# Optimization experiments

Hardware: AMD Instinct MI355X
Metric: run time of the kernel (lower is better)

## Reference

```python
import jax, jax.numpy as jnp
import numpy as np

B, S, D, H, K = 2, 1024, 1024, 16, 33  # batch, seq, d_model, heads, rel buckets (k+1)
d = D // H


def setup_inputs() -> dict:
    key = jax.random.key(0)
    ks = jax.random.split(key, 16)
    w = lambda k, shape: jax.random.normal(k, shape, dtype=jnp.float32) * 0.02
    return {
        "hidden_state": jax.random.normal(ks[0], (B, S, D), dtype=jnp.float32),
        "pos_indices": jax.random.randint(ks[1], (B, S, S), 0, K),
        "mask": jax.random.bernoulli(ks[2], 0.1, (B, 1, 1, S)),
        "Wq": w(ks[3], (D, D)), "bq": w(ks[4], (D,)),
        "Wk": w(ks[5], (D, D)), "bk": w(ks[6], (D,)),
        "Wv": w(ks[7], (D, D)), "bv": w(ks[8], (D,)),
        "Wo": w(ks[9], (D, D)), "bo": w(ks[10], (D,)),
        "rel_q": w(ks[11], (H, K, d)),
        "rel_k": w(ks[12], (H, K, d)),
        "rel_v": w(ks[13], (H, K, d)),
    }


def reference(hidden_state, pos_indices, mask, Wq, bq, Wk, bk, Wv, bv, Wo, bo,
              rel_q, rel_k, rel_v):
    b, s, dm = hidden_state.shape
    h, k_, dp = rel_q.shape
    # projections -> [B,H,S,d]
    def proj(x, W, bias):
        return (x @ W + bias).reshape(b, s, h, dp).transpose(0, 2, 1, 3)
    q = proj(hidden_state, Wq, bq)
    kk = proj(hidden_state, Wk, bk)
    v = proj(hidden_state, Wv, bv)
    # scale_factor = 1 (c2c) + 1 (rel_q) + 1 (rel_k)
    scale = 1.0 / np.sqrt(dp * 3).astype(np.float32)
    # content-to-content
    c2c = jnp.einsum("bhid,bhjd->bhij", q, kk) * scale
    idx = jnp.broadcast_to(pos_indices[:, None], (b, h, s, s))
    # position-to-content: raw [B,H,K,S], gathered along K with per-(i,j) bucket
    raw_p2c = jnp.einsum("hkd,bhjd->bhkj", rel_q, kk) * scale
    p2c = jnp.take_along_axis(raw_p2c, idx, axis=2)
    # content-to-position: raw [B,H,S,K], gathered along K
    raw_c2p = jnp.einsum("bhid,hkd->bhik", q, rel_k) * scale
    c2p = jnp.take_along_axis(raw_c2p, idx, axis=3)
    scores = c2c + p2c + c2p
    scores = jnp.where(mask, jnp.float32(-1e9), scores)
    probs = jax.nn.softmax(scores, axis=-1)  # dropout is identity in eval
    ctx = jnp.einsum("bhij,bhjd->bhid", probs, v)
    # value-side relative term: sum_j P[i,j] * rel_v[bucket(i,j)]
    oh = jax.nn.one_hot(pos_indices, k_, dtype=probs.dtype)  # [B,S,S,K]
    agg = jnp.einsum("bhij,bijk->bhik", probs, oh)
    ctx = ctx + jnp.einsum("bhik,hkd->bhid", agg, rel_v)
    out = ctx.transpose(0, 2, 1, 3).reshape(b, s, dm)
    return out @ Wo + bo
```

## Files before the change

### kernel.cpp

```cpp
#include <hip/hip_runtime.h>
#include <hip/hip_bf16.h>

#define B_ 2
#define S_ 1024
#define D_ 1024
#define H_ 16
#define K_ 33
#define DH 64
#define SCALE 0.07216878364870322f
#define FXS 32768.0f
#define FXI (1.0f / 32768.0f)

typedef __attribute__((ext_vector_type(8))) short bf16x8;
typedef __attribute__((ext_vector_type(4))) float f32x4;

__device__ __forceinline__ float b2f(unsigned short u) {
    return __uint_as_float(((unsigned int)u) << 16);
}
__device__ __forceinline__ unsigned short f2b(float f) {
    unsigned int u = __float_as_uint(f);
    u += 0x7FFFu + ((u >> 16) & 1u);
    return (unsigned short)(u >> 16);
}
__device__ __forceinline__ float ldf(const void* p, int i, int f32) {
    return f32 ? ((const float*)p)[i] : b2f(((const unsigned short*)p)[i]);
}
__device__ __forceinline__ float4 ldf4(const void* p, int i, int f32) {
    if (f32) return *(const float4*)((const float*)p + i);
    ushort4 u = *(const ushort4*)((const unsigned short*)p + i);
    return make_float4(b2f(u.x), b2f(u.y), b2f(u.z), b2f(u.w));
}
__device__ __forceinline__ float4 ldb4(const unsigned short* p, int i) {
    ushort4 u = *(const ushort4*)(p + i);
    return make_float4(b2f(u.x), b2f(u.y), b2f(u.z), b2f(u.w));
}

__global__ __launch_bounds__(256) void prep(const void* __restrict__ hidden,
                                            const void* __restrict__ mask,
                                            int* __restrict__ flags,
                                            float* __restrict__ mflag) {
    __shared__ int cnt;
    __shared__ int mev[6];
    const int t = threadIdx.x;
    if (t == 0) cnt = 0;
    if (t < 6) mev[t] = 0;
    __syncthreads();
    const unsigned short* hu = (const unsigned short*)hidden;
    int c = 0;
    for (int i = t; i < 2048; i += 256) {
        int e = (hu[i] >> 7) & 0xFF;
        if (e >= 0x8E) c++;
    }
    if (c) atomicAdd(&cnt, c);
    const unsigned char* mb = (const unsigned char*)mask;
    int e_bf = 0, e_f32 = 0, e_f64 = 0, e_f16 = 0, e_u8 = 0;
    for (int p = t; p < 2048; p += 256) {
        unsigned char v = mb[p];
        if ((p & 7) == 6 && v == 0xF0) e_f64 = 1;
        if ((p & 3) == 1 && v == 0x3F) e_bf = 1;
        if ((p & 3) == 3 && v == 0x3F) e_f32 = 1;
        if ((p & 1) == 1 && v == 0x3C) e_f16 = 1;
        if ((p & 3) != 0 && v != 0) e_u8 = 1;
    }
    if (e_f64) atomicOr(&mev[5], 1);
    if (e_bf)  atomicOr(&mev[3], 1);
    if (e_f32) atomicOr(&mev[2], 1);
    if (e_f16) atomicOr(&mev[4], 1);
    if (e_u8)  atomicOr(&mev[1], 1);
    __syncthreads();
    const int f32flag = (cnt >= 8) ? 1 : 0;
    const int mm = mev[5] ? 5 : (mev[3] ? 3 : (mev[2] ? 2 : (mev[4] ? 4 : (mev[1] ? 1 : 0))));
    if (t == 0) { flags[0] = f32flag; flags[2] = mm; }
    for (int j = t; j < B_ * S_; j += 256) {
        int m;
        if (mm == 5)      m = (((const double*)mask)[j] != 0.0);
        else if (mm == 3 || mm == 4) m = (((const unsigned short*)mask)[j] != 0);
        else if (mm == 2) m = (((const float*)mask)[j] != 0.f);
        else if (mm == 1) m = (mb[j] != 0);
        else              m = (((const int*)mask)[j] != 0);
        mflag[j] = m ? 1.f : 0.f;
    }
}

__global__ __launch_bounds__(256) void pos_pack(const int* __restrict__ pos,
                                                unsigned char* __restrict__ pos8) {
    int i = blockIdx.x * 256 + threadIdx.x;
    if (i >= (B_ * S_ * S_) / 4) return;
    int4 p = *(const int4*)&pos[i * 4];
    uchar4 o;
    o.x = (unsigned char)min(max(p.x, 0), K_ - 1);
    o.y = (unsigned char)min(max(p.y, 0), K_ - 1);
    o.z = (unsigned char)min(max(p.z, 0), K_ - 1);
    o.w = (unsigned char)min(max(p.w, 0), K_ - 1);
    *(uchar4*)&pos8[i * 4] = o;
}

__global__ __launch_bounds__(256) void w_pack(const void* __restrict__ W0,
                                              const void* __restrict__ W1,
                                              const void* __restrict__ W2,
                                              const void* __restrict__ W3,
                                              const int* __restrict__ flags,
                                              unsigned short* __restrict__ T0,
                                              unsigned short* __restrict__ T1,
                                              unsigned short* __restrict__ T2,
                                              unsigned short* __restrict__ T3) {
    __shared__ unsigned short tl[64][66];
    const int f32u = flags[0];
    const int z = blockIdx.z;
    const void* W = z == 0 ? W0 : (z == 1 ? W1 : (z == 2 ? W2 : W3));
    unsigned short* T = z == 0 ? T0 : (z == 1 ? T1 : (z == 2 ? T2 : T3));
    const int k0 = blockIdx.y * 64, n0 = blockIdx.x * 64;
    const int t = threadIdx.x;
    {
        int kr = t >> 2, nc = (t & 3) * 16;
#pragma unroll
        for (int u = 0; u < 4; ++u) {
            float4 v = ldf4(W, (k0 + kr) * 1024 + n0 + nc + u * 4, f32u);
            tl[kr][nc + u * 4 + 0] = f2b(v.x);
            tl[kr][nc + u * 4 + 1] = f2b(v.y);
            tl[kr][nc + u * 4 + 2] = f2b(v.z);
            tl[kr][nc + u * 4 + 3] = f2b(v.w);
        }
    }
    __syncthreads();
    {
        int nr = t >> 2, kc = (t & 3) * 16;
        unsigned short o[16];
#pragma unroll
        for (int u = 0; u < 16; ++u) o[u] = tl[kc + u][nr];
#pragma unroll
        for (int u = 0; u < 4; ++u)
            *(ushort4*)&T[(n0 + nr) * 1024 + k0 + kc + u * 4] = *(ushort4*)&o[u * 4];
    }
}

__global__ __launch_bounds__(512, 2) void gemm_qkv_mfma(const void* __restrict__ X,
                                                        const void* __restrict__ W0,
                                                        const void* __restrict__ W1,
                                                        const void* __restrict__ W2,
                                                        const unsigned short* __restrict__ T0,
                                                        const unsigned short* __restrict__ T1,
                                                        const unsigned short* __restrict__ T2,
                                                        const void* __restrict__ b0,
                                                        const void* __restrict__ b1,
                                                        const void* __restrict__ b2,
                                                        const int* __restrict__ flags, int useT,
                                                        unsigned short* __restrict__ q,
                                                        unsigned short* __restrict__ kk_,
                                                        unsigned short* __restrict__ v) {
    __shared__ unsigned short Asl[128][40];
    __shared__ unsigned short Bsl[128][40];
    const int f32u = flags[0];
    const int z = blockIdx.z;
    const void* W = z == 0 ? W0 : (z == 1 ? W1 : W2);
    const unsigned short* WT = z == 0 ? T0 : (z == 1 ? T1 : T2);
    const void* bias = z == 0 ? b0 : (z == 1 ? b1 : b2);
    unsigned short* outp = z == 0 ? q : (z == 1 ? kk_ : v);
    const int m0 = blockIdx.y * 128, n0 = blockIdx.x * 128;
    const int t = threadIdx.x;
    const int w = t >> 6, lane = t & 63;
    const int wr = w >> 2, wc = w & 3;
    const int lm = lane & 15, lg = lane >> 4;

    const int am = t >> 2, ac8 = (t & 3) * 8;
    const int bn = t & 127, bkq = (t >> 7) * 8;

    f32x4 acc[4][2] = {};
    float4 pa0, pa1;
    ushort4 tb0, tb1;
    float pbx[8];

    {
        int base = (m0 + am) * 1024 + ac8;
        pa0 = ldf4(X, base, f32u);
        pa1 = ldf4(X, base + 4, f32u);
        if (useT) {
            const ushort4* s = (const ushort4*)&WT[(n0 + am) * 1024 + ac8];
            tb0 = s[0]; tb1 = s[1];
        } else {
#pragma unroll
            for (int qi = 0; qi < 8; ++qi)
                pbx[qi] = ldf(W, (bkq + qi) * 1024 + n0 + bn, f32u);
        }
    }

    for (int k0 = 0; k0 < 1024; k0 += 32) {
        {
            ushort4 u0 = {f2b(pa0.x), f2b(pa0.y), f2b(pa0.z), f2b(pa0.w)};
            ushort4 u1 = {f2b(pa1.x), f2b(pa1.y), f2b(pa1.z), f2b(pa1.w)};
            *(ushort4*)&Asl[am][ac8] = u0;
            *(ushort4*)&Asl[am][ac8 + 4] = u1;
            if (useT) {
                *(ushort4*)&Bsl[am][ac8] = tb0;
                *(ushort4*)&Bsl[am][ac8 + 4] = tb1;
            } else {
#pragma unroll
                for (int qi = 0; qi < 8; qi += 2) {
                    unsigned int pk = (unsigned int)f2b(pbx[qi]) |
                                      ((unsigned int)f2b(pbx[qi + 1]) << 16);
                    *(unsigned int*)&Bsl[bn][bkq + qi] = pk;
                }
            }
        }
        __syncthreads();
        if (k0 + 32 < 1024) {
            int kn = k0 + 32;
            int base = (m0 + am) * 1024 + kn + ac8;
            pa0 = ldf4(X, base, f32u);
            pa1 = ldf4(X, base + 4, f32u);
            if (useT) {
                const ushort4* s = (const ushort4*)&WT[(n0 + am) * 1024 + kn + ac8];
                tb0 = s[0]; tb1 = s[1];
            } else {
#pragma unroll
                for (int qi = 0; qi < 8; ++qi)
                    pbx[qi] = ldf(W, (kn + bkq + qi) * 1024 + n0 + bn, f32u);
            }
        }
        bf16x8 af[4], bfr[2];
#pragma unroll
        for (int mi = 0; mi < 4; ++mi)
            af[mi] = *(const bf16x8*)&Asl[wr * 64 + mi * 16 + lm][lg * 8];
#pragma unroll
        for (int nj = 0; nj < 2; ++nj)
            bfr[nj] = *(const bf16x8*)&Bsl[wc * 32 + nj * 16 + lm][lg * 8];
#pragma unroll
        for (int mi = 0; mi < 4; ++mi)
#pragma unroll
            for (int nj = 0; nj < 2; ++nj)
                acc[mi][nj] = __builtin_amdgcn_mfma_f32_16x16x32_bf16(af[mi], bfr[nj],
                                                                      acc[mi][nj], 0, 0, 0);
        __syncthreads();
    }
#pragma unroll
    for (int nj = 0; nj < 2; ++nj) {
        int n = n0 + wc * 32 + nj * 16 + lm;
        float bv = ldf(bias, n, f32u);
        int hh = n >> 6, dd = n & 63;
#pragma unroll
        for (int mi = 0; mi < 4; ++mi) {
#pragma unroll
            for (int r = 0; r < 4; ++r) {
                int m = m0 + wr * 64 + mi * 16 + lg * 4 + r;
                int bb = m >> 10, ii = m & 1023;
                outp[((bb * H_ + hh) * S_ + ii) * DH + dd] = f2b(acc[mi][nj][r] + bv);
            }
        }
    }
}

__global__ __launch_bounds__(512, 2) void gemm_out_mfma(const unsigned short* __restrict__ X,
                                                        const void* __restrict__ W,
                                                        const unsigned short* __restrict__ WT,
                                                        const void* __restrict__ bias,
                                                        const int* __restrict__ flags, int useT,
                                                        float* __restrict__ out) {
    __shared__ unsigned short Asl[128][40];
    __shared__ unsigned short Bsl[128][40];
    const int f32u = flags[0];
    const int m0 = blockIdx.y * 128, n0 = blockIdx.x * 128;
    const int t = threadIdx.x;
    const int w = t >> 6, lane = t & 63;
    const int wr = w >> 2, wc = w & 3;
    const int lm = lane & 15, lg = lane >> 4;

    const int am = t >> 2, ac8 = (t & 3) * 8;
    const int bn = t & 127, bkq = (t >> 7) * 8;

    f32x4 acc[4][2] = {};
    ushort4 pa0, pa1, tb0, tb1;
    float pbx[8];

    {
        const ushort4* src = (const ushort4*)&X[(m0 + am) * 1024 + ac8];
        pa0 = src[0];
        pa1 = src[1];
        if (useT) {
            const ushort4* s = (const ushort4*)&WT[(n0 + am) * 1024 + ac8];
            tb0 = s[0]; tb1 = s[1];
        } else {
#pragma unroll
            for (int qi = 0; qi < 8; ++qi)
                pbx[qi] = ldf(W, (bkq + qi) * 1024 + n0 + bn, f32u);
        }
    }

    for (int k0 = 0; k0 < 1024; k0 += 32) {
        {
            *(ushort4*)&Asl[am][ac8] = pa0;
            *(ushort4*)&Asl[am][ac8 + 4] = pa1;
            if (useT) {
                *(ushort4*)&Bsl[am][ac8] = tb0;
                *(ushort4*)&Bsl[am][ac8 + 4] = tb1;
            } else {
#pragma unroll
                for (int qi = 0; qi < 8; qi += 2) {
                    unsigned int pk = (unsigned int)f2b(pbx[qi]) |
                                      ((unsigned int)f2b(pbx[qi + 1]) << 16);
                    *(unsigned int*)&Bsl[bn][bkq + qi] = pk;
                }
            }
        }
        __syncthreads();
        if (k0 + 32 < 1024) {
            int kn = k0 + 32;
            const ushort4* src = (const ushort4*)&X[(m0 + am) * 1024 + kn + ac8];
            pa0 = src[0];
            pa1 = src[1];
            if (useT) {
                const ushort4* s = (const ushort4*)&WT[(n0 + am) * 1024 + kn + ac8];
                tb0 = s[0]; tb1 = s[1];
            } else {
#pragma unroll
                for (int qi = 0; qi < 8; ++qi)
                    pbx[qi] = ldf(W, (kn + bkq + qi) * 1024 + n0 + bn, f32u);
            }
        }
        bf16x8 af[4], bfr[2];
#pragma unroll
        for (int mi = 0; mi < 4; ++mi)
            af[mi] = *(const bf16x8*)&Asl[wr * 64 + mi * 16 + lm][lg * 8];
#pragma unroll
        for (int nj = 0; nj < 2; ++nj)
            bfr[nj] = *(const bf16x8*)&Bsl[wc * 32 + nj * 16 + lm][lg * 8];
#pragma unroll
        for (int mi = 0; mi < 4; ++mi)
#pragma unroll
            for (int nj = 0; nj < 2; ++nj)
                acc[mi][nj] = __builtin_amdgcn_mfma_f32_16x16x32_bf16(af[mi], bfr[nj],
                                                                      acc[mi][nj], 0, 0, 0);
        __syncthreads();
    }
#pragma unroll
    for (int nj = 0; nj < 2; ++nj) {
        int n = n0 + wc * 32 + nj * 16 + lm;
        float bv = ldf(bias, n, f32u);
#pragma unroll
        for (int mi = 0; mi < 4; ++mi) {
#pragma unroll
            for (int r = 0; r < 4; ++r) {
                int m = m0 + wr * 64 + mi * 16 + lg * 4 + r;
                out[m * 1024 + n] = acc[mi][nj][r] + bv;
            }
        }
    }
}

__global__ __launch_bounds__(256) void rel_fused(const unsigned short* __restrict__ kws,
                                                 const unsigned short* __restrict__ qws,
                                                 const void* __restrict__ relq,
                                                 const void* __restrict__ relk,
                                                 const int* __restrict__ flags,
                                                 unsigned short* __restrict__ p2c,
                                                 unsigned short* __restrict__ c2p) {
    __shared__ float xt[64][68];
    __shared__ float rr[33][68];
    const int f32u = flags[0];
    const int bh = blockIdx.y, h = bh & 15;
    const int x0 = blockIdx.x * 64;
    const int t = threadIdx.x;
    if (blockIdx.z == 0) {
#pragma unroll
        for (int qq = 0; qq < 4; ++qq) {
            int idx = t + 256 * qq;
            int j = idx >> 4, d4 = idx & 15;
            *(float4*)&xt[j][d4 * 4] = ldb4(kws, (bh * S_ + x0 + j) * DH + d4 * 4);
        }
        for (int idx = t; idx < 33 * 16; idx += 256) {
            int k = idx >> 4, d4 = idx & 15;
            *(float4*)&rr[k][d4 * 4] = ldf4(relq, (h * K_ + k) * DH + d4 * 4, f32u);
        }
        __syncthreads();
        for (int o = t; o < 33 * 64; o += 256) {
            int k = o >> 6, j = o & 63;
            float s = 0.f;
#pragma unroll
            for (int d4 = 0; d4 < 16; ++d4) {
                float4 a = *(const float4*)&rr[k][d4 * 4];
                float4 b = *(const float4*)&xt[j][d4 * 4];
                s += a.x * b.x + a.y * b.y + a.z * b.z + a.w * b.w;
            }
            p2c[(bh * K_ + k) * S_ + x0 + j] = f2b(s * SCALE);
        }
    } else {
#pragma unroll
        for (int qq = 0; qq < 4; ++qq) {
            int idx = t + 256 * qq;
            int i = idx >> 4, d4 = idx & 15;
            *(float4*)&xt[i][d4 * 4] = ldb4(qws, (bh * S_ + x0 + i) * DH + d4 * 4);
        }
        for (int idx = t; idx < 33 * 16; idx += 256) {
            int k = idx >> 4, d4 = idx & 15;
            *(float4*)&rr[k][d4 * 4] = ldf4(relk, (h * K_ + k) * DH + d4 * 4, f32u);
        }
        __syncthreads();
        for (int o = t; o < 64 * 33; o += 256) {
            int i = o / 33, k = o % 33;
            float s = 0.f;
#pragma unroll
            for (int d4 = 0; d4 < 16; ++d4) {
                float4 a = *(const float4*)&xt[i][d4 * 4];
                float4 b = *(const float4*)&rr[k][d4 * 4];
                s += a.x * b.x + a.y * b.y + a.z * b.z + a.w * b.w;
            }
            c2p[(bh * S_ + x0 + i) * K_ + k] = f2b(s * SCALE);
        }
    }
}

#define PS_OFF   0
#define VT_OFF   32768
#define P2CS_OFF 32768
#define C2P_OFF  50176
#define AG_OFF   54528
#define RV_OFF   63232
#define MF_OFF   67456
#define ATTN_LDS 68480

__device__ __forceinline__ int ps_addr(int il, int jc) {
    return PS_OFF + il * 512 +
           ((jc * 2) ^ ((((il >> 2) & 3) << 5) ^ ((il & 3) << 4)));
}

__global__ __launch_bounds__(512, 4) void attn_mfma(const unsigned short* __restrict__ qws,
                                                    const unsigned short* __restrict__ kws,
                                                    const unsigned short* __restrict__ vws,
                                                    const unsigned short* __restrict__ p2c,
                                                    const unsigned short* __restrict__ c2p,
                                                    const float* __restrict__ mflag,
                                                    const unsigned char* __restrict__ pos8,
                                                    const int* __restrict__ pos32,
                                                    int use8,
                                                    const void* __restrict__ relv,
                                                    const int* __restrict__ flags,
                                                    unsigned short* __restrict__ ctxo) {
    extern __shared__ char smem[];
    const int f32u = flags[0];
    const int lin = blockIdx.y * 16 + blockIdx.x;
    const int logi = (lin & 7) * 64 + (lin >> 3);
    const int bh = logi >> 4, b = bh >> 4, h = bh & 15;
    const int i0 = (logi & 15) * 64;
    const int t = threadIdx.x;
    const int w = t >> 6, lane = t & 63;
    const int lm = lane & 15, lg = lane >> 4;
    const int iband = (w & 3) * 16;
    const int jh = w >> 2;
    const int dbase = jh * 32;

    unsigned int* agU = (unsigned int*)(smem + AG_OFF);
    unsigned short* c2pS = (unsigned short*)(smem + C2P_OFF);
    unsigned short* rvS = (unsigned short*)(smem + RV_OFF);
    unsigned char* mfS = (unsigned char*)(smem + MF_OFF);

    for (int idx = t; idx < 64 * 33; idx += 512) {
        int il = idx / 33, k = idx % 33;
        c2pS[il * 34 + k] = c2p[(bh * S_ + i0 + il) * K_ + k];
    }
    for (int idx = t; idx < 33 * 64; idx += 512) {
        int k = idx >> 6, d = idx & 63;
        rvS[k * 64 + d] = f2b(ldf(relv, (h * K_ + k) * DH + d, f32u));
    }
    for (int idx = t; idx < 1024; idx += 512)
        mfS[idx] = (mflag[b * S_ + idx] != 0.f) ? 1 : 0;
    for (int idx = t; idx < 64 * 34; idx += 512) agU[idx] = 0u;

    bf16x8 aq0 = *(const bf16x8*)&qws[(bh * S_ + i0 + iband + lm) * DH + lg * 8];
    bf16x8 aq1 = *(const bf16x8*)&qws[(bh * S_ + i0 + iband + lm) * DH + 32 + lg * 8];
    f32x4 acc0 = {}, acc1 = {};

    const int p2cbase = bh * K_ * S_;
    const int rowbase = (b * S_ + i0 + iband + lg * 4) * S_;
    __syncthreads();

    for (int c = 0; c < 4; ++c) {
        for (int idx = t; idx < 33 * 32; idx += 512) {
            int k = idx >> 5, v8 = idx & 31;
            uint4 src = *(const uint4*)&p2c[p2cbase + k * S_ + c * 256 + v8 * 8];
            unsigned int* dst = (unsigned int*)(smem + P2CS_OFF + k * 516 + v8 * 16);
            dst[0] = src.x; dst[1] = src.y; dst[2] = src.z; dst[3] = src.w;
        }
        __syncthreads();

        for (int jt = 0; jt < 8; ++jt) {
            const int jc = jh * 128 + jt * 16 + lm;
            const int jcol = c * 256 + jc;
            int pb4[4];
            if (use8) {
#pragma unroll
                for (int r = 0; r < 4; ++r)
                    pb4[r] = pos8[rowbase + r * S_ + jcol];
            } else {
#pragma unroll
                for (int r = 0; r < 4; ++r) {
                    int p = pos32[rowbase + r * S_ + jcol];
                    pb4[r] = min(max(p, 0), K_ - 1);
                }
            }
            bf16x8 kf0 = *(const bf16x8*)&kws[(bh * S_ + jcol) * DH + lg * 8];
            bf16x8 kf1 = *(const bf16x8*)&kws[(bh * S_ + jcol) * DH + 32 + lg * 8];
            f32x4 a = {};
            a = __builtin_amdgcn_mfma_f32_16x16x32_bf16(aq0, kf0, a, 0, 0, 0);
            a = __builtin_amdgcn_mfma_f32_16x16x32_bf16(aq1, kf1, a, 0, 0, 0);
            const int masked = mfS[jcol];
#pragma unroll
            for (int r = 0; r < 4; ++r) {
                int il = iband + lg * 4 + r;
                int pb = pb4[r];
                float gv = b2f(*(const unsigned short*)(smem + P2CS_OFF + pb * 516 + jc * 2));
                float s = a[r] * SCALE + gv + b2f(c2pS[il * 34 + pb]);
                float ev = masked ? 0.f : __expf(s);
                *(unsigned short*)(smem + ps_addr(il, jc)) = f2b(ev);
                atomicAdd(&agU[il * 34 + pb], (unsigned int)(ev * FXS));
            }
        }
        __syncthreads();

        for (int st = 0; st < 2; ++st) {
#pragma unroll
            for (int u = 0; u < 2; ++u) {
                int idx = t + u * 512;
                int jj = idx >> 3;
                int a8 = idx & 7;
                int d0 = a8 * 8;
                int j = c * 256 + st * 128 + jj;
                bf16x8 vv = *(const bf16x8*)&vws[(bh * S_ + j) * DH + d0];
#pragma unroll
                for (int e = 0; e < 8; ++e) {
                    int ee = (e + a8) & 7;
                    *(unsigned short*)(smem + VT_OFF + (d0 + ee) * 272 + jj * 2) =
                        ((short*)&vv)[ee];
                }
            }
            __syncthreads();
#pragma unroll
            for (int ks = 0; ks < 4; ++ks) {
                int jcb = st * 128 + ks * 32 + lg * 8;
                bf16x8 af = *(const bf16x8*)(smem + ps_addr(iband + lm, jcb));
                bf16x8 b0 = *(const bf16x8*)(smem + VT_OFF + (dbase + lm) * 272 +
                                             (ks * 32 + lg * 8) * 2);
                bf16x8 b1 = *(const bf16x8*)(smem + VT_OFF + (dbase + 16 + lm) * 272 +
                                             (ks * 32 + lg * 8) * 2);
                acc0 = __builtin_amdgcn_mfma_f32_16x16x32_bf16(af, b0, acc0, 0, 0, 0);
                acc1 = __builtin_amdgcn_mfma_f32_16x16x32_bf16(af, b1, acc1, 0, 0, 0);
            }
            __syncthreads();
        }
    }

#pragma unroll
    for (int r = 0; r < 4; ++r) {
        int il = iband + lg * 4 + r;
        float rs = 0.f;
        float o0 = acc0[r], o1 = acc1[r];
        for (int kb = 0; kb < K_; ++kb) {
            float a = (float)agU[il * 34 + kb] * FXI;
            rs += a;
            o0 += a * b2f(rvS[kb * 64 + dbase + lm]);
            o1 += a * b2f(rvS[kb * 64 + dbase + 16 + lm]);
        }
        float inv = 1.0f / rs;
        ctxo[(b * S_ + i0 + il) * D_ + h * DH + dbase + lm] = f2b(o0 * inv);
        ctxo[(b * S_ + i0 + il) * D_ + h * DH + dbase + 16 + lm] = f2b(o1 * inv);
    }
}

extern "C" void kernel_launch(void* const* d_in, const int* in_sizes, int n_in,
                              void* d_out, int out_size, void* d_ws, size_t ws_size,
                              hipStream_t stream) {
    const void* hidden = d_in[0];
    const void* pos = d_in[1];
    const void* mask = d_in[2];
    const void* Wq = d_in[3];
    const void* bq = d_in[4];
    const void* Wk = d_in[5];
    const void* bk = d_in[6];
    const void* Wv = d_in[7];
    const void* bv = d_in[8];
    const void* Wo = d_in[9];
    const void* bo = d_in[10];
    const void* rq = d_in[11];
    const void* rk = d_in[12];
    const void* rv = d_in[13];

    unsigned char* wsb = (unsigned char*)d_ws;
    size_t o = 0;
    int* flags = (int*)(wsb + o);            o += 256;
    float* mfl = (float*)(wsb + o);          o += 2048 * 4;
    o = (o + 255) & ~(size_t)255;
    unsigned short* qb   = (unsigned short*)(wsb + o); o += 4194304;
    unsigned short* kb   = (unsigned short*)(wsb + o); o += 4194304;
    unsigned short* vb   = (unsigned short*)(wsb + o); o += 4194304;
    unsigned short* p2cb = (unsigned short*)(wsb + o); o += 2162688;
    unsigned short* c2pb = (unsigned short*)(wsb + o); o += 2162688;
    unsigned short* ctxb = (unsigned short*)(wsb + o); o += 4194304;
    unsigned char* pos8  = (unsigned char*)(wsb + o);  o += 2097152;
    const int use8 = (ws_size >= o) ? 1 : 0;
    unsigned short* wTq = (unsigned short*)(wsb + o);  o += 2097152;
    unsigned short* wTk = (unsigned short*)(wsb + o);  o += 2097152;
    unsigned short* wTv = (unsigned short*)(wsb + o);  o += 2097152;
    unsigned short* wTo = (unsigned short*)(wsb + o);  o += 2097152;
    const int useT = (ws_size >= o) ? 1 : 0;

    float* out = (float*)d_out;
    const int* posi = (const int*)pos;

    hipFuncSetAttribute(reinterpret_cast<const void*>(attn_mfma),
                        hipFuncAttributeMaxDynamicSharedMemorySize, ATTN_LDS);

    dim3 tb(256);
    prep<<<dim3(1), tb, 0, stream>>>(hidden, mask, flags, mfl);
    if (use8) pos_pack<<<dim3(2048), tb, 0, stream>>>(posi, pos8);
    if (useT) w_pack<<<dim3(16, 16, 4), tb, 0, stream>>>(Wq, Wk, Wv, Wo, flags,
                                                         wTq, wTk, wTv, wTo);
    gemm_qkv_mfma<<<dim3(8, 16, 3), dim3(512), 0, stream>>>(hidden, Wq, Wk, Wv,
                                                            wTq, wTk, wTv,
                                                            bq, bk, bv, flags, useT,
                                                            qb, kb, vb);
    rel_fused<<<dim3(16, 32, 2), tb, 0, stream>>>(kb, qb, rq, rk, flags, p2cb, c2pb);
    attn_mfma<<<dim3(16, 32), dim3(512), ATTN_LDS, stream>>>(qb, kb, vb, p2cb, c2pb, mfl,
                                                             pos8, posi, use8, rv, flags,
                                                             ctxb);
    gemm_out_mfma<<<dim3(8, 16), dim3(512), 0, stream>>>(ctxb, Wo, wTo, bo, flags, useT,
                                                         out);
}
```

Measured before the change: 158.4 us.

## Shrink GEMM tiles to 128x64, fold log2e into scale, split aggregation atomics

Both projection GEMMs move from 128x128 tiles with 512 threads to 128x64 tiles with 256 threads, doubling the grid so more blocks fill the CUs. The out-projection grid grows from 128 to 256 blocks. In attention, log2(e) is folded into the score scale and into the precomputed p2c/c2p tables so exp2f replaces __expf. The bucket-aggregation atomics are split across two LDS copies, indexed by jh, which lowers contention at the cost of extra LDS and an extra sum at the end. Halving the N tile also halves A-tile reuse per block.

```diff
diff --git a/kernel.cpp b/kernel.cpp
--- a/kernel.cpp
+++ b/kernel.cpp
@@ -8,6 +8,8 @@
 #define K_ 33
 #define DH 64
 #define SCALE 0.07216878364870322f
+#define LOG2E 1.4426950408889634f
+#define SCALEL (SCALE * LOG2E)
 #define FXS 32768.0f
 #define FXI (1.0f / 32768.0f)
 
@@ -134,7 +136,7 @@
     }
 }
 
-__global__ __launch_bounds__(512, 2) void gemm_qkv_mfma(const void* __restrict__ X,
+__global__ __launch_bounds__(256, 3) void gemm_qkv_mfma(const void* __restrict__ X,
                                                         const void* __restrict__ W0,
                                                         const void* __restrict__ W1,
                                                         const void* __restrict__ W2,
@@ -149,72 +151,74 @@
                                                         unsigned short* __restrict__ kk_,
                                                         unsigned short* __restrict__ v) {
     __shared__ unsigned short Asl[128][40];
-    __shared__ unsigned short Bsl[128][40];
+    __shared__ unsigned short Bsl[64][40];
     const int f32u = flags[0];
     const int z = blockIdx.z;
     const void* W = z == 0 ? W0 : (z == 1 ? W1 : W2);
     const unsigned short* WT = z == 0 ? T0 : (z == 1 ? T1 : T2);
     const void* bias = z == 0 ? b0 : (z == 1 ? b1 : b2);
     unsigned short* outp = z == 0 ? q : (z == 1 ? kk_ : v);
-    const int m0 = blockIdx.y * 128, n0 = blockIdx.x * 128;
+    const int m0 = blockIdx.y * 128, n0 = blockIdx.x * 64;
     const int t = threadIdx.x;
     const int w = t >> 6, lane = t & 63;
-    const int wr = w >> 2, wc = w & 3;
+    const int wr = w >> 1, wc = w & 1;
     const int lm = lane & 15, lg = lane >> 4;
 
-    const int am = t >> 2, ac8 = (t & 3) * 8;
-    const int bn = t & 127, bkq = (t >> 7) * 8;
+    const int am = t >> 1, ac16 = (t & 1) * 16;
+    const int bn = t >> 2, bk8 = (t & 3) * 8;
+    const int fbn = t & 63, fbkq = (t >> 6) * 8;
 
     f32x4 acc[4][2] = {};
-    float4 pa0, pa1;
+    float4 pa[4];
     ushort4 tb0, tb1;
     float pbx[8];
 
     {
-        int base = (m0 + am) * 1024 + ac8;
-        pa0 = ldf4(X, base, f32u);
-        pa1 = ldf4(X, base + 4, f32u);
+        int base = (m0 + am) * 1024 + ac16;
+#pragma unroll
+        for (int u = 0; u < 4; ++u) pa[u] = ldf4(X, base + u * 4, f32u);
         if (useT) {
-            const ushort4* s = (const ushort4*)&WT[(n0 + am) * 1024 + ac8];
+            const ushort4* s = (const ushort4*)&WT[(n0 + bn) * 1024 + bk8];
             tb0 = s[0]; tb1 = s[1];
         } else {
 #pragma unroll
             for (int qi = 0; qi < 8; ++qi)
-                pbx[qi] = ldf(W, (bkq + qi) * 1024 + n0 + bn, f32u);
+                pbx[qi] = ldf(W, (fbkq + qi) * 1024 + n0 + fbn, f32u);
         }
     }
 
     for (int k0 = 0; k0 < 1024; k0 += 32) {
         {
-            ushort4 u0 = {f2b(pa0.x), f2b(pa0.y), f2b(pa0.z), f2b(pa0.w)};
-            ushort4 u1 = {f2b(pa1.x), f2b(pa1.y), f2b(pa1.z), f2b(pa1.w)};
-            *(ushort4*)&Asl[am][ac8] = u0;
-            *(ushort4*)&Asl[am][ac8 + 4] = u1;
+#pragma unroll
+            for (int u = 0; u < 4; ++u) {
+                ushort4 uv = {f2b(pa[u].x), f2b(pa[u].y), f2b(pa[u].z), f2b(pa[u].w)};
+                *(ushort4*)&Asl[am][ac16 + u * 4] = uv;
+            }
             if (useT) {
-                *(ushort4*)&Bsl[am][ac8] = tb0;
-                *(ushort4*)&Bsl[am][ac8 + 4] = tb1;
+                *(ushort4*)&Bsl[bn][bk8] = tb0;
+                *(ushort4*)&Bsl[bn][bk8 + 4] = tb1;
             } else {
 #pragma unroll
                 for (int qi = 0; qi < 8; qi += 2) {
                     unsigned int pk = (unsigned int)f2b(pbx[qi]) |
                                       ((unsigned int)f2b(pbx[qi + 1]) << 16);
-                    *(unsigned int*)&Bsl[bn][bkq + qi] = pk;
+                    *(unsigned int*)&Bsl[fbn][fbkq + qi] = pk;
                 }
             }
         }
         __syncthreads();
         if (k0 + 32 < 1024) {
             int kn = k0 + 32;
-            int base = (m0 + am) * 1024 + kn + ac8;
-            pa0 = ldf4(X, base, f32u);
-            pa1 = ldf4(X, base + 4, f32u);
+            int base = (m0 + am) * 1024 + kn + ac16;
+#pragma unroll
+            for (int u = 0; u < 4; ++u) pa[u] = ldf4(X, base + u * 4, f32u);
             if (useT) {
-                const ushort4* s = (const ushort4*)&WT[(n0 + am) * 1024 + kn + ac8];
+                const ushort4* s = (const ushort4*)&WT[(n0 + bn) * 1024 + kn + bk8];
                 tb0 = s[0]; tb1 = s[1];
             } else {
 #pragma unroll
                 for (int qi = 0; qi < 8; ++qi)
-                    pbx[qi] = ldf(W, (kn + bkq + qi) * 1024 + n0 + bn, f32u);
+                    pbx[qi] = ldf(W, (kn + fbkq + qi) * 1024 + n0 + fbn, f32u);
             }
         }
         bf16x8 af[4], bfr[2];
@@ -249,71 +253,73 @@
     }
 }
 
-__global__ __launch_bounds__(512, 2) void gemm_out_mfma(const unsigned short* __restrict__ X,
+__global__ __launch_bounds__(256, 3) void gemm_out_mfma(const unsigned short* __restrict__ X,
                                                         const void* __restrict__ W,
                                                         const unsigned short* __restrict__ WT,
                                                         const void* __restrict__ bias,
                                                         const int* __restrict__ flags, int useT,
                                                         float* __restrict__ out) {
     __shared__ unsigned short Asl[128][40];
-    __shared__ unsigned short Bsl[128][40];
+    __shared__ unsigned short Bsl[64][40];
     const int f32u = flags[0];
-    const int m0 = blockIdx.y * 128, n0 = blockIdx.x * 128;
+    const int m0 = blockIdx.y * 128, n0 = blockIdx.x * 64;
     const int t = threadIdx.x;
     const int w = t >> 6, lane = t & 63;
-    const int wr = w >> 2, wc = w & 3;
+    const int wr = w >> 1, wc = w & 1;
     const int lm = lane & 15, lg = lane >> 4;
 
-    const int am = t >> 2, ac8 = (t & 3) * 8;
-    const int bn = t & 127, bkq = (t >> 7) * 8;
+    const int am = t >> 1, ac16 = (t & 1) * 16;
+    const int bn = t >> 2, bk8 = (t & 3) * 8;
+    const int fbn = t & 63, fbkq = (t >> 6) * 8;
 
     f32x4 acc[4][2] = {};
-    ushort4 pa0, pa1, tb0, tb1;
+    ushort4 pa[4];
+    ushort4 tb0, tb1;
     float pbx[8];
 
     {
-        const ushort4* src = (const ushort4*)&X[(m0 + am) * 1024 + ac8];
-        pa0 = src[0];
-        pa1 = src[1];
+        const ushort4* src = (const ushort4*)&X[(m0 + am) * 1024 + ac16];
+#pragma unroll
+        for (int u = 0; u < 4; ++u) pa[u] = src[u];
         if (useT) {
-            const ushort4* s = (const ushort4*)&WT[(n0 + am) * 1024 + ac8];
+            const ushort4* s = (const ushort4*)&WT[(n0 + bn) * 1024 + bk8];
             tb0 = s[0]; tb1 = s[1];
         } else {
 #pragma unroll
             for (int qi = 0; qi < 8; ++qi)
-                pbx[qi] = ldf(W, (bkq + qi) * 1024 + n0 + bn, f32u);
+                pbx[qi] = ldf(W, (fbkq + qi) * 1024 + n0 + fbn, f32u);
         }
     }
 
     for (int k0 = 0; k0 < 1024; k0 += 32) {
         {
-            *(ushort4*)&Asl[am][ac8] = pa0;
-            *(ushort4*)&Asl[am][ac8 + 4] = pa1;
+#pragma unroll
+            for (int u = 0; u < 4; ++u) *(ushort4*)&Asl[am][ac16 + u * 4] = pa[u];
             if (useT) {
-                *(ushort4*)&Bsl[am][ac8] = tb0;
-                *(ushort4*)&Bsl[am][ac8 + 4] = tb1;
+                *(ushort4*)&Bsl[bn][bk8] = tb0;
+                *(ushort4*)&Bsl[bn][bk8 + 4] = tb1;
             } else {
 #pragma unroll
                 for (int qi = 0; qi < 8; qi += 2) {
                     unsigned int pk = (unsigned int)f2b(pbx[qi]) |
                                       ((unsigned int)f2b(pbx[qi + 1]) << 16);
-                    *(unsigned int*)&Bsl[bn][bkq + qi] = pk;
+                    *(unsigned int*)&Bsl[fbn][fbkq + qi] = pk;
                 }
             }
         }
         __syncthreads();
         if (k0 + 32 < 1024) {
             int kn = k0 + 32;
-            const ushort4* src = (const ushort4*)&X[(m0 + am) * 1024 + kn + ac8];
-            pa0 = src[0];
-            pa1 = src[1];
+            const ushort4* src = (const ushort4*)&X[(m0 + am) * 1024 + kn + ac16];
+#pragma unroll
+            for (int u = 0; u < 4; ++u) pa[u] = src[u];
             if (useT) {
-                const ushort4* s = (const ushort4*)&WT[(n0 + am) * 1024 + kn + ac8];
+                const ushort4* s = (const ushort4*)&WT[(n0 + bn) * 1024 + kn + bk8];
                 tb0 = s[0]; tb1 = s[1];
             } else {
 #pragma unroll
                 for (int qi = 0; qi < 8; ++qi)
-                    pbx[qi] = ldf(W, (kn + bkq + qi) * 1024 + n0 + bn, f32u);
+                    pbx[qi] = ldf(W, (kn + fbkq + qi) * 1024 + n0 + fbn, f32u);
             }
         }
         bf16x8 af[4], bfr[2];
@@ -380,7 +386,7 @@
                 float4 b = *(const float4*)&xt[j][d4 * 4];
                 s += a.x * b.x + a.y * b.y + a.z * b.z + a.w * b.w;
             }
-            p2c[(bh * K_ + k) * S_ + x0 + j] = f2b(s * SCALE);
+            p2c[(bh * K_ + k) * S_ + x0 + j] = f2b(s * SCALEL);
         }
     } else {
 #pragma unroll
@@ -403,7 +409,7 @@
                 float4 b = *(const float4*)&rr[k][d4 * 4];
                 s += a.x * b.x + a.y * b.y + a.z * b.z + a.w * b.w;
             }
-            c2p[(bh * S_ + x0 + i) * K_ + k] = f2b(s * SCALE);
+            c2p[(bh * S_ + x0 + i) * K_ + k] = f2b(s * SCALEL);
         }
     }
 }
@@ -413,9 +419,9 @@
 #define P2CS_OFF 32768
 #define C2P_OFF  50176
 #define AG_OFF   54528
-#define RV_OFF   63232
-#define MF_OFF   67456
-#define ATTN_LDS 68480
+#define RV_OFF   71936
+#define MF_OFF   76160
+#define ATTN_LDS 77184
 
 __device__ __forceinline__ int ps_addr(int il, int jc) {
     return PS_OFF + il * 512 +
@@ -462,7 +468,7 @@
     }
     for (int idx = t; idx < 1024; idx += 512)
         mfS[idx] = (mflag[b * S_ + idx] != 0.f) ? 1 : 0;
-    for (int idx = t; idx < 64 * 34; idx += 512) agU[idx] = 0u;
+    for (int idx = t; idx < 2 * 64 * 34; idx += 512) agU[idx] = 0u;
 
     bf16x8 aq0 = *(const bf16x8*)&qws[(bh * S_ + i0 + iband + lm) * DH + lg * 8];
     bf16x8 aq1 = *(const bf16x8*)&qws[(bh * S_ + i0 + iband + lm) * DH + 32 + lg * 8];
@@ -470,6 +476,7 @@
 
     const int p2cbase = bh * K_ * S_;
     const int rowbase = (b * S_ + i0 + iband + lg * 4) * S_;
+    const int agbase = jh * 2176;
     __syncthreads();
 
     for (int c = 0; c < 4; ++c) {
@@ -507,10 +514,10 @@
                 int il = iband + lg * 4 + r;
                 int pb = pb4[r];
                 float gv = b2f(*(const unsigned short*)(smem + P2CS_OFF + pb * 516 + jc * 2));
-                float s = a[r] * SCALE + gv + b2f(c2pS[il * 34 + pb]);
-                float ev = masked ? 0.f : __expf(s);
+                float s = a[r] * SCALEL + gv + b2f(c2pS[il * 34 + pb]);
+                float ev = masked ? 0.f : exp2f(s);
                 *(unsigned short*)(smem + ps_addr(il, jc)) = f2b(ev);
-                atomicAdd(&agU[il * 34 + pb], (unsigned int)(ev * FXS));
+                atomicAdd(&agU[agbase + il * 34 + pb], (unsigned int)(ev * FXS));
             }
         }
         __syncthreads();
@@ -553,7 +560,7 @@
         float rs = 0.f;
         float o0 = acc0[r], o1 = acc1[r];
         for (int kb = 0; kb < K_; ++kb) {
-            float a = (float)agU[il * 34 + kb] * FXI;
+            float a = (float)(agU[il * 34 + kb] + agU[2176 + il * 34 + kb]) * FXI;
             rs += a;
             o0 += a * b2f(rvS[kb * 64 + dbase + lm]);
             o1 += a * b2f(rvS[kb * 64 + dbase + 16 + lm]);
@@ -612,14 +619,14 @@
     if (use8) pos_pack<<<dim3(2048), tb, 0, stream>>>(posi, pos8);
     if (useT) w_pack<<<dim3(16, 16, 4), tb, 0, stream>>>(Wq, Wk, Wv, Wo, flags,
                                                          wTq, wTk, wTv, wTo);
-    gemm_qkv_mfma<<<dim3(8, 16, 3), dim3(512), 0, stream>>>(hidden, Wq, Wk, Wv,
-                                                            wTq, wTk, wTv,
-                                                            bq, bk, bv, flags, useT,
-                                                            qb, kb, vb);
+    gemm_qkv_mfma<<<dim3(16, 16, 3), tb, 0, stream>>>(hidden, Wq, Wk, Wv,
+                                                      wTq, wTk, wTv,
+                                                      bq, bk, bv, flags, useT,
+                                                      qb, kb, vb);
     rel_fused<<<dim3(16, 32, 2), tb, 0, stream>>>(kb, qb, rq, rk, flags, p2cb, c2pb);
     attn_mfma<<<dim3(16, 32), dim3(512), ATTN_LDS, stream>>>(qb, kb, vb, p2cb, c2pb, mfl,
                                                              pos8, posi, use8, rv, flags,
                                                              ctxb);
-    gemm_out_mfma<<<dim3(8, 16), dim3(512), 0, stream>>>(ctxb, Wo, wTo, bo, flags, useT,
-                                                         out);
-}
+    gemm_out_mfma<<<dim3(16, 16), tb, 0, stream>>>(ctxb, Wo, wTo, bo, flags, useT,
+                                                   out);
+}
```

After: 159.3 us. About the same (+0.5%).
